# Kernel optimization log

Hardware: AMD Instinct MI355X
Metric: run time of the kernel (lower is better)

Reference implementation:

```python
import jax, jax.numpy as jnp
import numpy as np

EPS = 1e-5   # BatchNorm eps
SF = 2       # scale_factor
K = 5        # up_kernel


def setup_inputs() -> dict:
    key = jax.random.key(0)
    ks = jax.random.split(key, 8)
    return {
        "x": jax.random.normal(ks[0], (4, 128, 64, 64), jnp.float32),
        "comp_w": jax.random.normal(ks[1], (64, 128), jnp.float32) * 0.05,   # 1x1 conv weight (O,I)
        "bn_gamma": 1.0 + 0.1 * jax.random.normal(ks[2], (64,), jnp.float32),
        "bn_beta": 0.1 * jax.random.normal(ks[3], (64,), jnp.float32),
        "bn_mean": 0.1 * jax.random.normal(ks[4], (64,), jnp.float32),
        "bn_var": jax.random.uniform(ks[5], (64,), jnp.float32, minval=0.5, maxval=1.5),
        "enc_w": jax.random.normal(ks[6], (100, 64, 3, 3), jnp.float32) * 0.05,  # K*K*SF*SF=100 out ch
        "enc_b": jax.random.normal(ks[7], (100,), jnp.float32) * 0.05,
    }


def reference(x, comp_w, bn_gamma, bn_beta, bn_mean, bn_var, enc_w, enc_b):
    b, c, h, w = x.shape
    k2 = K * K
    # channel compressor: 1x1 conv + BatchNorm (inference) + SiLU
    y = jnp.einsum('bchw,oc->bohw', x, comp_w)
    inv = bn_gamma / jnp.sqrt(bn_var + EPS)
    y = y * inv[None, :, None, None] + (bn_beta - bn_mean * inv)[None, :, None, None]
    y = y * jax.nn.sigmoid(y)  # SiLU
    # content encoder: 3x3 conv, SAME padding, bias
    m = jax.lax.conv_general_dilated(
        y, enc_w, window_strides=(1, 1), padding='SAME',
        dimension_numbers=('NCHW', 'OIHW', 'NCHW')) + enc_b[None, :, None, None]
    # pixel shuffle with r=SF: channels viewed as (k2, SF, SF)
    m = m.reshape(b, k2, SF, SF, h, w)
    m = m.transpose(0, 1, 4, 2, 5, 3).reshape(b, k2, h * SF, w * SF)
    m = jax.nn.softmax(m, axis=1)  # normalize over the k*k kernel positions
    # nearest-neighbor upsample of x
    xu = jnp.repeat(jnp.repeat(x, SF, axis=2), SF, axis=3)
    p = K // 2
    xp = jnp.pad(xu, ((0, 0), (0, 0), (p, p), (p, p)))
    H, W = h * SF, w * SF
    # fused reassembly: sum over 25 static kernel offsets (same math as
    # unfold(k=5,pad=2) * softmax(mask) summed over dim=2, without the huge
    # (b,c,25,H,W) intermediate)
    out = jnp.zeros((b, c, H, W), x.dtype)
    for ki in range(K):
        for kj in range(K):
            out = out + xp[:, :, ki:ki + H, kj:kj + W] * m[:, ki * K + kj][:, None]
    return out
```

## Files before the change

kernel.cpp:

```cpp
#include <hip/hip_runtime.h>
#include <hip/hip_bf16.h>

#define BN 4
#define CIN 128
#define CMID 64
#define HH 64
#define WW 64
#define HW 4096
#define K2 25
#define H2 128
#define W2 128
#define HW2 16384
#define EPSN 1e-5f

typedef __attribute__((ext_vector_type(8))) short short8;
typedef __attribute__((ext_vector_type(4))) float f32x4;

__device__ inline unsigned short f2b(float f) {
  union { __hip_bfloat16 h; unsigned short u; } cv;
  cv.h = __float2bfloat16(f);
  return cv.u;
}

__device__ inline float b16f(unsigned s) {
  union { unsigned u; float f; } cv;
  cv.u = s << 16;
  return cv.f;
}

__global__ void pack_w_kernel(const float* __restrict__ ew,
                              const float* __restrict__ cw,
                              unsigned short* __restrict__ Wb,
                              unsigned short* __restrict__ Wc) {
  int i = blockIdx.x * 256 + threadIdx.x;
  if (i < 9 * 128 * 64) {
    int c = i & 63;
    int n = (i >> 6) & 127;
    int tap = i >> 13;
    int q = n >> 5, k = n & 31;
    float v = (k < K2) ? ew[((k * 4 + q) * CMID + c) * 9 + tap] : 0.f;
    Wb[i] = f2b(v);
  } else if (i < 9 * 128 * 64 + 8192) {
    int j = i - 9 * 128 * 64;
    int e = j & 7;
    int lanepos = (j >> 3) & 63;
    int grp = j >> 9;
    int lm = lanepos & 15, lg = lanepos >> 4;
    int ks = grp & 3, mt = grp >> 2;
    Wc[j] = f2b(cw[(mt * 16 + lm) * CIN + ks * 32 + lg * 8 + e]);
  }
}

__global__ __launch_bounds__(256) void fused_kernel(
    const float* __restrict__ x, const unsigned short* __restrict__ Wb,
    const unsigned short* __restrict__ Wc, const float* __restrict__ gamma,
    const float* __restrict__ beta, const float* __restrict__ mean,
    const float* __restrict__ var, const float* __restrict__ eb,
    float* __restrict__ out) {
  __shared__ unsigned short yl[3 * 20 * 64];
  __shared__ unsigned short xl[128 * 3 * 26];
  __shared__ float ml[128][17];
  __shared__ float q3s[16][37];
  __shared__ float sinv[CMID], sadd[CMID];
  int t = threadIdx.x;
  int bx = blockIdx.x;
  int b = bx >> 8;
  int rem = bx & 255;
  int h = rem >> 2;
  int p0g = (rem & 3) * 16;

  for (int i = t; i < 480; i += 256) {
    uint4 z; z.x = 0; z.y = 0; z.z = 0; z.w = 0;
    ((uint4*)yl)[i] = z;
  }
  if (t < CMID) {
    float iv = gamma[t] * rsqrtf(var[t] + EPSN);
    sinv[t] = iv;
    sadd[t] = beta[t] - mean[t] * iv;
  }
  for (int i = t; i < 128 * 3 * 6; i += 256) {
    int c = i / 18;
    int r = i - c * 18;
    int dh = r / 6, j4 = r - dh * 6;
    int hh = h + dh - 1;
    int cb = p0g - 4 + 4 * j4;
    float4 f; f.x = 0.f; f.y = 0.f; f.z = 0.f; f.w = 0.f;
    if ((unsigned)hh < (unsigned)HH) {
      const float* xp = &x[(size_t)(b * CIN + c) * HW + hh * WW];
      if (cb >= 0 && cb <= WW - 4) {
        f = *(const float4*)&xp[cb];
      } else {
        float tmp[4];
#pragma unroll
        for (int e = 0; e < 4; ++e)
          tmp[e] = ((unsigned)(cb + e) < (unsigned)WW) ? xp[cb + e] : 0.f;
        f.x = tmp[0]; f.y = tmp[1]; f.z = tmp[2]; f.w = tmp[3];
      }
    }
    char* dst = (char*)xl + (c * 3 + dh) * 52 + 8 * j4;
    *(unsigned*)dst = (unsigned)f2b(f.x) | ((unsigned)f2b(f.y) << 16);
    *(unsigned*)(dst + 4) = (unsigned)f2b(f.z) | ((unsigned)f2b(f.w) << 16);
  }
  __syncthreads();

  {
    int lane = t & 63;
    int nt = __builtin_amdgcn_readfirstlane(t >> 6);
    int lm = lane & 15, lg = lane >> 4;
    int p = nt * 16 + lm;
    int pc = (p < 54) ? p : 0;
    int dh = pc / 18, colw = pc - dh * 18;
    int lc = colw + 3;

    short8 bfr[4];
#pragma unroll
    for (int ks = 0; ks < 4; ++ks) {
      unsigned short tmp[8];
#pragma unroll
      for (int j = 0; j < 8; ++j) {
        int c = ks * 32 + lg * 8 + j;
        tmp[j] = *(const unsigned short*)((const char*)xl + (c * 3 + dh) * 52 +
                                          2 * lc);
      }
      bfr[ks] = *(short8*)tmp;
    }

    f32x4 acc[4];
#pragma unroll
    for (int mt = 0; mt < 4; ++mt) acc[mt] = (f32x4){0.f, 0.f, 0.f, 0.f};
#pragma unroll
    for (int mt = 0; mt < 4; ++mt)
#pragma unroll
      for (int ks = 0; ks < 4; ++ks) {
        short8 af = *(const short8*)&Wc[(((mt * 4 + ks) << 6) + lane) * 8];
        acc[mt] = __builtin_amdgcn_mfma_f32_16x16x32_bf16(af, bfr[ks], acc[mt], 0, 0, 0);
      }

    int hh = h + dh - 1, wgc = p0g - 1 + colw;
    if (p < 54 && (unsigned)hh < (unsigned)HH && (unsigned)wgc < (unsigned)WW) {
      int R = dh * 20 + colw;
      int yxor = (R & 7) << 4;
#pragma unroll
      for (int mt = 0; mt < 4; ++mt) {
        int ob = mt * 16 + lg * 4;
        unsigned short pk[4];
#pragma unroll
        for (int r = 0; r < 4; ++r) {
          int o = ob + r;
          float v = acc[mt][r] * sinv[o] + sadd[o];
          v = v / (1.f + __expf(-v));
          pk[r] = f2b(v);
        }
        *(unsigned long long*)((char*)yl + R * 128 + ((ob * 2) ^ yxor)) =
            *(unsigned long long*)pk;
      }
    }
  }
  __syncthreads();

  {
    int lane = t & 63;
    int nq = __builtin_amdgcn_readfirstlane(t >> 6);
    int lm = lane & 15, lg = lane >> 4;

    f32x4 acc[2];
    acc[0] = (f32x4){0.f, 0.f, 0.f, 0.f};
    acc[1] = (f32x4){0.f, 0.f, 0.f, 0.f};

#pragma unroll
    for (int dh = 0; dh < 3; ++dh) {
#pragma unroll
      for (int dw = 0; dw < 3; ++dw) {
        int tap = dh * 3 + dw;
        int R = dh * 20 + lm + dw;
        char* rowp = (char*)yl + R * 128;
        int xorm = (R & 7) << 4;
        short8 a0 = *(short8*)(rowp + ((lg * 16) ^ xorm));
        short8 a1 = *(short8*)(rowp + ((64 + lg * 16) ^ xorm));
        const unsigned short* wt = Wb + tap * 8192 + lg * 8;
#pragma unroll
        for (int nti = 0; nti < 2; ++nti) {
          const unsigned short* bp = wt + ((nq * 2 + nti) * 16 + lm) * 64;
          short8 b0 = *(const short8*)bp;
          short8 b1 = *(const short8*)(bp + 32);
          acc[nti] = __builtin_amdgcn_mfma_f32_16x16x32_bf16(a0, b0, acc[nti], 0, 0, 0);
          acc[nti] = __builtin_amdgcn_mfma_f32_16x16x32_bf16(a1, b1, acc[nti], 0, 0, 0);
        }
      }
    }

#pragma unroll
    for (int nti = 0; nti < 2; ++nti)
#pragma unroll
      for (int r = 0; r < 4; ++r)
        ml[(nq * 2 + nti) * 16 + lm][lg * 4 + r] = acc[nti][r];
  }
  __syncthreads();

  if (t < 64) {
    int wl = t & 15, q = t >> 4;
    int wg = p0g + wl;
    int sh = q >> 1, sw = q & 1;
    float a25[K2];
#pragma unroll
    for (int k = 0; k < K2; ++k) a25[k] = ml[q * 32 + k][wl] + eb[k * 4 + q];

    float mx = a25[0];
#pragma unroll
    for (int k = 1; k < K2; ++k) mx = fmaxf(mx, a25[k]);
    float ssum = 0.f;
#pragma unroll
    for (int k = 0; k < K2; ++k) {
      a25[k] = __expf(a25[k] - mx);
      ssum += a25[k];
    }
    float inv = 1.f / ssum;

    float rs[3][5];
    if (sh == 0) {
#pragma unroll
      for (int j = 0; j < 5; ++j) {
        rs[0][j] = a25[j] + a25[5 + j];
        rs[1][j] = a25[10 + j] + a25[15 + j];
        rs[2][j] = a25[20 + j];
      }
    } else {
#pragma unroll
      for (int j = 0; j < 5; ++j) {
        rs[0][j] = a25[j];
        rs[1][j] = a25[5 + j] + a25[10 + j];
        rs[2][j] = a25[15 + j] + a25[20 + j];
      }
    }
    float q3[3][3];
#pragma unroll
    for (int i = 0; i < 3; ++i) {
      if (sw == 0) {
        q3[i][0] = rs[i][0] + rs[i][1];
        q3[i][1] = rs[i][2] + rs[i][3];
        q3[i][2] = rs[i][4];
      } else {
        q3[i][0] = rs[i][0];
        q3[i][1] = rs[i][1] + rs[i][2];
        q3[i][2] = rs[i][3] + rs[i][4];
      }
      q3[i][0] *= inv;
      q3[i][1] *= inv;
      q3[i][2] *= inv;
    }
    if (h == 0) { q3[0][0] = q3[0][1] = q3[0][2] = 0.f; }
    if (h == HH - 1) { q3[2][0] = q3[2][1] = q3[2][2] = 0.f; }
    if (wg == 0) { q3[0][0] = q3[1][0] = q3[2][0] = 0.f; }
    if (wg == WW - 1) { q3[0][2] = q3[1][2] = q3[2][2] = 0.f; }

#pragma unroll
    for (int i = 0; i < 3; ++i)
#pragma unroll
      for (int j = 0; j < 3; ++j) q3s[wl][q * 9 + i * 3 + j] = q3[i][j];
  }
  __syncthreads();

  {
    int wl = t & 15;
    int sh = (t >> 4) & 1;
    int cg = t >> 5;

    float m0[9], m1[9];
#pragma unroll
    for (int j = 0; j < 9; ++j) {
      m0[j] = q3s[wl][(2 * sh) * 9 + j];
      m1[j] = q3s[wl][(2 * sh + 1) * 9 + j];
    }

    int lcE = (wl + 3) & ~1;
    bool oddw = (wl & 1) != 0;

    float* ob = out + (size_t)(b * CIN + cg * 16) * HW2 +
                (size_t)(2 * h + sh) * W2 + 2 * (p0g + wl);

    for (int cp = 0; cp < 16; ++cp) {
      int c = cg * 16 + cp;
      const char* xrow = (const char*)xl + (size_t)(c * 3) * 52;
      float xv[9];
#pragma unroll
      for (int rr = 0; rr < 3; ++rr) {
        unsigned a = *(const unsigned*)(xrow + rr * 52 + 2 * lcE);
        unsigned bb = *(const unsigned*)(xrow + rr * 52 + 2 * lcE + 4);
        unsigned s0, s1, s2;
        if (oddw) {
          s0 = a & 0xffffu; s1 = a >> 16; s2 = bb & 0xffffu;
        } else {
          s0 = a >> 16; s1 = bb & 0xffffu; s2 = bb >> 16;
        }
        xv[rr * 3 + 0] = b16f(s0);
        xv[rr * 3 + 1] = b16f(s1);
        xv[rr * 3 + 2] = b16f(s2);
      }
      float o0 = 0.f, o1 = 0.f;
#pragma unroll
      for (int j = 0; j < 9; ++j) {
        o0 += m0[j] * xv[j];
        o1 += m1[j] * xv[j];
      }
      float2 st = {o0, o1};
      *(float2*)&ob[(size_t)cp * HW2] = st;
    }
  }
}

extern "C" void kernel_launch(void* const* d_in, const int* in_sizes, int n_in,
                              void* d_out, int out_size, void* d_ws, size_t ws_size,
                              hipStream_t stream) {
  const float* x = (const float*)d_in[0];
  const float* cw = (const float*)d_in[1];
  const float* gamma = (const float*)d_in[2];
  const float* beta = (const float*)d_in[3];
  const float* mean = (const float*)d_in[4];
  const float* var = (const float*)d_in[5];
  const float* ew = (const float*)d_in[6];
  const float* eb = (const float*)d_in[7];
  float* out = (float*)d_out;

  unsigned short* Wb = (unsigned short*)d_ws;
  unsigned short* Wc = Wb + (size_t)73728;

  pack_w_kernel<<<320, 256, 0, stream>>>(ew, cw, Wb, Wc);
  fused_kernel<<<BN * HH * 4, 256, 0, stream>>>(x, Wb, Wc, gamma, beta, mean, var,
                                                eb, out);
}
```

Baseline: 43.13 us.

## Split compressor into separate kernel writing bf16 y to workspace, drop halo recompute

The 1x1 compressor conv with BN and SiLU moves out of the fused kernel into its own kernel. That kernel also packs the encoder weights and writes y in bf16, pixel-major, to the workspace. The main kernel then loads y tiles with halo from global memory instead of recomputing the compressor for 54 halo positions per block, which was about 3.4x redundant MFMA work. This costs an extra global round trip for y and gives up some fusion. It also trims the ml shared buffer to 100 rows and reuses yl's memory for q3s.

```diff
diff --git a/kernel.cpp b/kernel.cpp
--- a/kernel.cpp
+++ b/kernel.cpp
@@ -28,40 +28,80 @@
   return cv.f;
 }
 
-__global__ void pack_w_kernel(const float* __restrict__ ew,
-                              const float* __restrict__ cw,
-                              unsigned short* __restrict__ Wb,
-                              unsigned short* __restrict__ Wc) {
-  int i = blockIdx.x * 256 + threadIdx.x;
-  if (i < 9 * 128 * 64) {
+__global__ __launch_bounds__(256) void compress_kernel(
+    const float* __restrict__ x, const float* __restrict__ cw,
+    const float* __restrict__ gamma, const float* __restrict__ beta,
+    const float* __restrict__ mean, const float* __restrict__ var,
+    const float* __restrict__ ew, unsigned short* __restrict__ Wb,
+    unsigned short* __restrict__ yt) {
+  __shared__ unsigned short xT[16 * 136];
+  __shared__ float sinv[CMID], sadd[CMID];
+  int t = threadIdx.x;
+  int bx = blockIdx.x;
+  int b = bx >> 8;
+  int rem = bx & 255;
+  int h = rem >> 2;
+  int w0 = (rem & 3) * 16;
+
+  if (t < 72) {
+    int i = bx * 72 + t;
     int c = i & 63;
     int n = (i >> 6) & 127;
     int tap = i >> 13;
     int q = n >> 5, k = n & 31;
     float v = (k < K2) ? ew[((k * 4 + q) * CMID + c) * 9 + tap] : 0.f;
     Wb[i] = f2b(v);
-  } else if (i < 9 * 128 * 64 + 8192) {
-    int j = i - 9 * 128 * 64;
-    int e = j & 7;
-    int lanepos = (j >> 3) & 63;
-    int grp = j >> 9;
-    int lm = lanepos & 15, lg = lanepos >> 4;
-    int ks = grp & 3, mt = grp >> 2;
-    Wc[j] = f2b(cw[(mt * 16 + lm) * CIN + ks * 32 + lg * 8 + e]);
-  }
-}
-
-__global__ __launch_bounds__(256) void fused_kernel(
+  }
+  if (t < CMID) {
+    float iv = gamma[t] * rsqrtf(var[t] + EPSN);
+    sinv[t] = iv;
+    sadd[t] = beta[t] - mean[t] * iv;
+  }
+  for (int i = t; i < 512; i += 256) {
+    int c = i >> 2;
+    int w4 = (i & 3) * 4;
+    float4 f = *(const float4*)&x[(size_t)(b * CIN + c) * HW + h * WW + w0 + w4];
+    xT[(w4 + 0) * 136 + c] = f2b(f.x);
+    xT[(w4 + 1) * 136 + c] = f2b(f.y);
+    xT[(w4 + 2) * 136 + c] = f2b(f.z);
+    xT[(w4 + 3) * 136 + c] = f2b(f.w);
+  }
+  __syncthreads();
+
+  int lane = t & 63;
+  int nt = __builtin_amdgcn_readfirstlane(t >> 6);
+  int lm = lane & 15, lg = lane >> 4;
+
+  f32x4 acc = (f32x4){0.f, 0.f, 0.f, 0.f};
+#pragma unroll
+  for (int ks = 0; ks < 4; ++ks) {
+    short8 bf = *(const short8*)&xT[lm * 136 + ks * 32 + lg * 8];
+    short8 af;
+    const float* cp = &cw[(nt * 16 + lm) * CIN + ks * 32 + lg * 8];
+#pragma unroll
+    for (int e = 0; e < 8; ++e) af[e] = (short)f2b(cp[e]);
+    acc = __builtin_amdgcn_mfma_f32_16x16x32_bf16(af, bf, acc, 0, 0, 0);
+  }
+
+  int o0 = nt * 16 + lg * 4;
+  unsigned long long pk = 0;
+#pragma unroll
+  for (int r = 0; r < 4; ++r) {
+    float v = acc[r] * sinv[o0 + r] + sadd[o0 + r];
+    v = v / (1.f + __expf(-v));
+    pk |= (unsigned long long)f2b(v) << (16 * r);
+  }
+  *(unsigned long long*)&yt[((size_t)(b * HH + h) * WW + w0 + lm) * CMID + o0] =
+      pk;
+}
+
+__global__ __launch_bounds__(256) void carafe_kernel(
     const float* __restrict__ x, const unsigned short* __restrict__ Wb,
-    const unsigned short* __restrict__ Wc, const float* __restrict__ gamma,
-    const float* __restrict__ beta, const float* __restrict__ mean,
-    const float* __restrict__ var, const float* __restrict__ eb,
+    const unsigned short* __restrict__ yt, const float* __restrict__ eb,
     float* __restrict__ out) {
-  __shared__ unsigned short yl[3 * 20 * 64];
   __shared__ unsigned short xl[128 * 3 * 26];
-  __shared__ float ml[128][17];
-  __shared__ float q3s[16][37];
-  __shared__ float sinv[CMID], sadd[CMID];
+  __shared__ __align__(16) unsigned short yl[3 * 20 * 64];
+  __shared__ float ml[100][17];
   int t = threadIdx.x;
   int bx = blockIdx.x;
   int b = bx >> 8;
@@ -69,15 +109,6 @@
   int h = rem >> 2;
   int p0g = (rem & 3) * 16;
 
-  for (int i = t; i < 480; i += 256) {
-    uint4 z; z.x = 0; z.y = 0; z.z = 0; z.w = 0;
-    ((uint4*)yl)[i] = z;
-  }
-  if (t < CMID) {
-    float iv = gamma[t] * rsqrtf(var[t] + EPSN);
-    sinv[t] = iv;
-    sadd[t] = beta[t] - mean[t] * iv;
-  }
   for (int i = t; i < 128 * 3 * 6; i += 256) {
     int c = i / 18;
     int r = i - c * 18;
@@ -101,60 +132,16 @@
     *(unsigned*)dst = (unsigned)f2b(f.x) | ((unsigned)f2b(f.y) << 16);
     *(unsigned*)(dst + 4) = (unsigned)f2b(f.z) | ((unsigned)f2b(f.w) << 16);
   }
-  __syncthreads();
-
-  {
-    int lane = t & 63;
-    int nt = __builtin_amdgcn_readfirstlane(t >> 6);
-    int lm = lane & 15, lg = lane >> 4;
-    int p = nt * 16 + lm;
-    int pc = (p < 54) ? p : 0;
-    int dh = pc / 18, colw = pc - dh * 18;
-    int lc = colw + 3;
-
-    short8 bfr[4];
-#pragma unroll
-    for (int ks = 0; ks < 4; ++ks) {
-      unsigned short tmp[8];
-#pragma unroll
-      for (int j = 0; j < 8; ++j) {
-        int c = ks * 32 + lg * 8 + j;
-        tmp[j] = *(const unsigned short*)((const char*)xl + (c * 3 + dh) * 52 +
-                                          2 * lc);
-      }
-      bfr[ks] = *(short8*)tmp;
-    }
-
-    f32x4 acc[4];
-#pragma unroll
-    for (int mt = 0; mt < 4; ++mt) acc[mt] = (f32x4){0.f, 0.f, 0.f, 0.f};
-#pragma unroll
-    for (int mt = 0; mt < 4; ++mt)
-#pragma unroll
-      for (int ks = 0; ks < 4; ++ks) {
-        short8 af = *(const short8*)&Wc[(((mt * 4 + ks) << 6) + lane) * 8];
-        acc[mt] = __builtin_amdgcn_mfma_f32_16x16x32_bf16(af, bfr[ks], acc[mt], 0, 0, 0);
-      }
-
-    int hh = h + dh - 1, wgc = p0g - 1 + colw;
-    if (p < 54 && (unsigned)hh < (unsigned)HH && (unsigned)wgc < (unsigned)WW) {
-      int R = dh * 20 + colw;
-      int yxor = (R & 7) << 4;
-#pragma unroll
-      for (int mt = 0; mt < 4; ++mt) {
-        int ob = mt * 16 + lg * 4;
-        unsigned short pk[4];
-#pragma unroll
-        for (int r = 0; r < 4; ++r) {
-          int o = ob + r;
-          float v = acc[mt][r] * sinv[o] + sadd[o];
-          v = v / (1.f + __expf(-v));
-          pk[r] = f2b(v);
-        }
-        *(unsigned long long*)((char*)yl + R * 128 + ((ob * 2) ^ yxor)) =
-            *(unsigned long long*)pk;
-      }
-    }
+  for (int i = t; i < 432; i += 256) {
+    int ch = i & 7;
+    int j = i >> 3;
+    int dh = j / 18, cwl = j - dh * 18;
+    int R = dh * 20 + cwl;
+    int hh = h + dh - 1, wg = p0g - 1 + cwl;
+    uint4 v; v.x = 0; v.y = 0; v.z = 0; v.w = 0;
+    if ((unsigned)hh < (unsigned)HH && (unsigned)wg < (unsigned)WW)
+      v = *(const uint4*)&yt[((size_t)(b * HH + hh) * WW + wg) * CMID + ch * 8];
+    *(uint4*)((char*)yl + R * 128 + ((ch * 16) ^ ((R & 7) << 4))) = v;
   }
   __syncthreads();
 
@@ -190,20 +177,25 @@
     }
 
 #pragma unroll
-    for (int nti = 0; nti < 2; ++nti)
-#pragma unroll
-      for (int r = 0; r < 4; ++r)
-        ml[(nq * 2 + nti) * 16 + lm][lg * 4 + r] = acc[nti][r];
+    for (int nti = 0; nti < 2; ++nti) {
+      int n = (nq * 2 + nti) * 16 + lm;
+      int k = n & 31, q = n >> 5;
+      if (k < K2) {
+#pragma unroll
+        for (int r = 0; r < 4; ++r) ml[k * 4 + q][lg * 4 + r] = acc[nti][r];
+      }
+    }
   }
   __syncthreads();
 
+  float* q3s = (float*)yl;
   if (t < 64) {
     int wl = t & 15, q = t >> 4;
     int wg = p0g + wl;
     int sh = q >> 1, sw = q & 1;
     float a25[K2];
 #pragma unroll
-    for (int k = 0; k < K2; ++k) a25[k] = ml[q * 32 + k][wl] + eb[k * 4 + q];
+    for (int k = 0; k < K2; ++k) a25[k] = ml[k * 4 + q][wl] + eb[k * 4 + q];
 
     float mx = a25[0];
 #pragma unroll
@@ -256,7 +248,7 @@
 #pragma unroll
     for (int i = 0; i < 3; ++i)
 #pragma unroll
-      for (int j = 0; j < 3; ++j) q3s[wl][q * 9 + i * 3 + j] = q3[i][j];
+      for (int j = 0; j < 3; ++j) q3s[wl * 37 + q * 9 + i * 3 + j] = q3[i][j];
   }
   __syncthreads();
 
@@ -268,8 +260,8 @@
     float m0[9], m1[9];
 #pragma unroll
     for (int j = 0; j < 9; ++j) {
-      m0[j] = q3s[wl][(2 * sh) * 9 + j];
-      m1[j] = q3s[wl][(2 * sh + 1) * 9 + j];
+      m0[j] = q3s[wl * 37 + (2 * sh) * 9 + j];
+      m1[j] = q3s[wl * 37 + (2 * sh + 1) * 9 + j];
     }
 
     int lcE = (wl + 3) & ~1;
@@ -322,9 +314,9 @@
   float* out = (float*)d_out;
 
   unsigned short* Wb = (unsigned short*)d_ws;
-  unsigned short* Wc = Wb + (size_t)73728;
-
-  pack_w_kernel<<<320, 256, 0, stream>>>(ew, cw, Wb, Wc);
-  fused_kernel<<<BN * HH * 4, 256, 0, stream>>>(x, Wb, Wc, gamma, beta, mean, var,
-                                                eb, out);
-}
+  unsigned short* yt = Wb + (size_t)73728;
+
+  compress_kernel<<<BN * HH * 4, 256, 0, stream>>>(x, cw, gamma, beta, mean,
+                                                   var, ew, Wb, yt);
+  carafe_kernel<<<BN * HH * 4, 256, 0, stream>>>(x, Wb, yt, eb, out);
+}
```

After: 44.48 us. +3.1%, slower.
